# Kernel tuning notes

Measured on AMD Instinct MI355X. Metric: run time of the kernel, lower is better.

The kernel has to match this reference:

```python
import jax, jax.numpy as jnp
import numpy as np

N_NODES = 100000
N_EDGES = 1600000
D = 64
NUM_HOPS = 3


def setup_inputs() -> dict:
    key = jax.random.key(0)
    ks = jax.random.split(key, 8)
    return {
        "H_l": jax.random.normal(ks[0], (N_NODES, D), dtype=jnp.float32),
        "edge_row": jax.random.randint(ks[1], (N_EDGES,), 0, N_NODES, dtype=jnp.int64),
        "edge_col": jax.random.randint(ks[2], (N_EDGES,), 0, N_NODES, dtype=jnp.int64),
        "edge_val": jax.random.uniform(ks[3], (N_EDGES,), dtype=jnp.float32),
        "out_degree": jax.random.uniform(ks[4], (N_NODES,), dtype=jnp.float32),
        "in_degree": jax.random.uniform(ks[5], (N_NODES,), dtype=jnp.float32),
        "hop_attention": jnp.ones((NUM_HOPS,), dtype=jnp.float32),
        "theta_out": jnp.full((NUM_HOPS,), 0.5, dtype=jnp.float32),
        "theta_in": jnp.full((NUM_HOPS,), 0.5, dtype=jnp.float32),
        "Theta": jax.random.normal(ks[6], (D, D), dtype=jnp.float32) * (6.0 ** 0.5) / (2 * D) ** 0.5,
    }


def reference(H_l, edge_row, edge_col, edge_val, out_degree, in_degree,
              hop_attention, theta_out, theta_in, Theta):
    n = H_l.shape[0]
    num_hops = hop_attention.shape[0]
    alpha = jax.nn.softmax(hop_attention)

    def spmm(rows, cols, X):
        # (A @ X)[r] = sum over edges (r,c): val * X[c]
        return jax.ops.segment_sum(edge_val[:, None] * X[cols], rows, num_segments=n)

    # fixed degree-scaled features (degrees clamped as in __init__)
    X_out = jnp.maximum(out_degree, 1e-8)[:, None] * H_l
    X_in = jnp.maximum(in_degree, 1e-8)[:, None] * H_l
    sum_term = jnp.zeros_like(H_l)
    for k in range(num_hops):
        # A^{k+1} @ (D_out H) computed by one more application of A per hop
        X_out = spmm(edge_row, edge_col, X_out)
        # (A^{k+1})^T @ (D_in H): transpose swaps row/col roles
        X_in = spmm(edge_col, edge_row, X_in)
        sum_term = sum_term + alpha[k] * (theta_out[k] * X_out + theta_in[k] * X_in)

    conv_term = jax.nn.sigmoid(sum_term @ Theta)
    return conv_term + H_l
```

## Files before the change

kernel.cpp:

```cpp
#include <hip/hip_runtime.h>
#include <hip/hip_fp16.h>

#define DFEAT 64
#define BKT_SHIFT 8
#define BKT_NODES 256
#define NBMAX 512
#define CH 4096
#define SRC_BITS 18
#define SRC_MASK ((1 << SRC_BITS) - 1)

__device__ __forceinline__ unsigned short f2h(float f) {
    return __half_as_ushort(__float2half(f));
}
__device__ __forceinline__ float h2f(unsigned short u) {
    return __half2float(__ushort_as_half(u));
}

__global__ void init_kernel(const float* __restrict__ H,
                            const float* __restrict__ outdeg,
                            const float* __restrict__ indeg,
                            const float* __restrict__ hop_att,
                            const float* __restrict__ th_out,
                            const float* __restrict__ th_in,
                            unsigned short* __restrict__ XAout,
                            unsigned short* __restrict__ XAin,
                            float* __restrict__ coefs, int n4) {
    int idx = blockIdx.x * blockDim.x + threadIdx.x;
    if (idx == 0) {
        float m = fmaxf(fmaxf(hop_att[0], hop_att[1]), hop_att[2]);
        float e0 = __expf(hop_att[0] - m);
        float e1 = __expf(hop_att[1] - m);
        float e2 = __expf(hop_att[2] - m);
        float inv = 1.0f / (e0 + e1 + e2);
        coefs[0] = e0 * inv * th_out[0]; coefs[1] = e0 * inv * th_in[0];
        coefs[2] = e1 * inv * th_out[1]; coefs[3] = e1 * inv * th_in[1];
        coefs[4] = e2 * inv * th_out[2]; coefs[5] = e2 * inv * th_in[2];
    }
    if (idx >= n4) return;
    int row = idx >> 4;
    float4 h = reinterpret_cast<const float4*>(H)[idx];
    float doo = fmaxf(outdeg[row], 1e-8f);
    float dii = fmaxf(indeg[row], 1e-8f);
    reinterpret_cast<ushort4*>(XAout)[idx] =
        make_ushort4(f2h(h.x * doo), f2h(h.y * doo), f2h(h.z * doo), f2h(h.w * doo));
    reinterpret_cast<ushort4*>(XAin)[idx] =
        make_ushort4(f2h(h.x * dii), f2h(h.y * dii), f2h(h.z * dii), f2h(h.w * dii));
}

__global__ __launch_bounds__(256) void hist2d_kernel(
        const int* __restrict__ erow, const int* __restrict__ ecol,
        int* __restrict__ cnt2, int nEdges, int nB, int nBlkA) {
    __shared__ int hR[NBMAX], hC[NBMAX];
    int k = blockIdx.x;
    for (int i = threadIdx.x; i < nB; i += 256) { hR[i] = 0; hC[i] = 0; }
    __syncthreads();
    int base = k * CH;
    int nV = min(CH, nEdges - base);
    for (int i = threadIdx.x; i < nV; i += 256) {
        atomicAdd(&hR[erow[base + i] >> BKT_SHIFT], 1);
        atomicAdd(&hC[ecol[base + i] >> BKT_SHIFT], 1);
    }
    __syncthreads();
    for (int b = threadIdx.x; b < nB; b += 256) {
        cnt2[(size_t)b * nBlkA + k] = hR[b];
        cnt2[((size_t)nB + b) * nBlkA + k] = hC[b];
    }
}

__global__ void scan_reduce1(const int* __restrict__ p, int* __restrict__ bsum,
                             int n) {
    int t = threadIdx.x, lane = t & 63, wid = t >> 6;
    int base = blockIdx.x * 1024 + t * 4;
    int s = 0;
#pragma unroll
    for (int i = 0; i < 4; ++i) { int idx = base + i; if (idx < n) s += p[idx]; }
#pragma unroll
    for (int o = 32; o >= 1; o >>= 1) s += __shfl_down(s, o, 64);
    __shared__ int wsum[4];
    if (lane == 0) wsum[wid] = s;
    __syncthreads();
    if (t == 0) bsum[blockIdx.x] = wsum[0] + wsum[1] + wsum[2] + wsum[3];
}

__global__ void scan_spine1(int* __restrict__ bsum, int nChunks) {
    int lane = threadIdx.x;
    int carry = 0;
    for (int base = 0; base < nChunks; base += 64) {
        int i = base + lane;
        int v = (i < nChunks) ? bsum[i] : 0;
        int s = v;
#pragma unroll
        for (int o = 1; o < 64; o <<= 1) {
            int x = __shfl_up(s, o, 64);
            if (lane >= o) s += x;
        }
        if (i < nChunks) bsum[i] = carry + s - v;
        carry += __shfl(s, 63, 64);
    }
}

__global__ void scan_down1(int* __restrict__ p, const int* __restrict__ bsum,
                           int n) {
    int t = threadIdx.x, lane = t & 63, wid = t >> 6;
    int base = blockIdx.x * 1024 + t * 4;
    int v[4];
    int tsum = 0;
#pragma unroll
    for (int i = 0; i < 4; ++i) {
        v[i] = (base + i < n) ? p[base + i] : 0;
        tsum += v[i];
    }
    int inc = tsum;
#pragma unroll
    for (int o = 1; o < 64; o <<= 1) {
        int x = __shfl_up(inc, o, 64);
        if (lane >= o) inc += x;
    }
    __shared__ int wsum[4];
    if (lane == 63) wsum[wid] = inc;
    __syncthreads();
    int woff = 0;
    for (int w = 0; w < wid; ++w) woff += wsum[w];
    int run = bsum[blockIdx.x] + woff + inc - tsum;
#pragma unroll
    for (int i = 0; i < 4; ++i) {
        if (base + i < n) p[base + i] = run;
        run += v[i];
    }
}

__global__ __launch_bounds__(256) void partA_kernel(
        const int* __restrict__ erow, const int* __restrict__ ecol,
        const float* __restrict__ eval, const int* __restrict__ base2,
        int2* __restrict__ recR, int2* __restrict__ recC,
        int nEdges, int nB, int nBlkA) {
    __shared__ int hist[NBMAX], scn[NBMAX], cur[NBMAX], gbase[NBMAX];
    __shared__ unsigned short keybuf[CH], slotKey[CH];
    __shared__ int2 stage[CH];
    int dir = blockIdx.y;
    const int* dk = dir ? ecol : erow;
    const int* ds = dir ? erow : ecol;
    int2* rec = dir ? recC : recR;
    int k = blockIdx.x;
    int base = k * CH;
    int nV = min(CH, nEdges - base);
    for (int i = threadIdx.x; i < nB; i += 256) {
        hist[i] = 0; cur[i] = 0;
        gbase[i] = base2[((size_t)dir * nB + i) * nBlkA + k] - dir * nEdges;
    }
    __syncthreads();
    for (int i = threadIdx.x; i < nV; i += 256) {
        int key = dk[base + i] >> BKT_SHIFT;
        keybuf[i] = (unsigned short)key;
        atomicAdd(&hist[key], 1);
    }
    __syncthreads();
    if (threadIdx.x < 64) {
        int lane = threadIdx.x;
        int carry = 0;
        for (int bb = 0; bb < nB; bb += 64) {
            int i = bb + lane;
            int v = (i < nB) ? hist[i] : 0;
            int s = v;
#pragma unroll
            for (int o = 1; o < 64; o <<= 1) {
                int x = __shfl_up(s, o, 64);
                if (lane >= o) s += x;
            }
            if (i < nB) scn[i] = carry + s - v;
            carry += __shfl(s, 63, 64);
        }
    }
    __syncthreads();
    for (int i = threadIdx.x; i < nV; i += 256) {
        int e = base + i;
        int key = keybuf[i];
        int slot = scn[key] + atomicAdd(&cur[key], 1);
        int dl = dk[e] & (BKT_NODES - 1);
        stage[slot] = make_int2(ds[e] | (dl << SRC_BITS), __float_as_int(eval[e]));
        slotKey[slot] = (unsigned short)key;
    }
    __syncthreads();
    for (int i = threadIdx.x; i < nV; i += 256) {
        int key = slotKey[i];
        rec[gbase[key] + (i - scn[key])] = stage[i];
    }
}

__global__ __launch_bounds__(256) void partB_kernel(
        const int2* __restrict__ recR, const int2* __restrict__ recC,
        const int* __restrict__ base2,
        int* __restrict__ rowptr, int* __restrict__ colptr,
        unsigned* __restrict__ pairsR, unsigned* __restrict__ pairsC,
        int nEdges, int nB, int nBlkA, int nNodes) {
    __shared__ int hist[BKT_NODES], scn[BKT_NODES], cur[BKT_NODES];
    int dir = blockIdx.y;
    int b = blockIdx.x;
    const int2* rec = dir ? recC : recR;
    unsigned* pairs = dir ? pairsC : pairsR;
    int* nptr = dir ? colptr : rowptr;
    int segB = base2[((size_t)dir * nB + b) * nBlkA] - dir * nEdges;
    int segE = (b == nB - 1) ? nEdges
             : base2[((size_t)dir * nB + b + 1) * nBlkA] - dir * nEdges;
    int t = threadIdx.x;
    hist[t] = 0; cur[t] = 0;
    __syncthreads();
    for (int j = segB + t; j < segE; j += 256)
        atomicAdd(&hist[(rec[j].x >> SRC_BITS) & (BKT_NODES - 1)], 1);
    __syncthreads();
    if (t < 64) {
        int lane = t, carry = 0;
        for (int bb = 0; bb < BKT_NODES; bb += 64) {
            int i = bb + lane;
            int v = hist[i], s = v;
#pragma unroll
            for (int o = 1; o < 64; o <<= 1) {
                int x = __shfl_up(s, o, 64);
                if (lane >= o) s += x;
            }
            scn[i] = carry + s - v;
            carry += __shfl(s, 63, 64);
        }
    }
    __syncthreads();
    int node = (b << BKT_SHIFT) + t;
    if (node < nNodes) nptr[node] = segB + scn[t];
    if (b == nB - 1 && t == 0) nptr[nNodes] = nEdges;
    for (int j = segB + t; j < segE; j += 256) {
        int2 r = rec[j];
        int dl = (r.x >> SRC_BITS) & (BKT_NODES - 1);
        int slot = segB + scn[dl] + atomicAdd(&cur[dl], 1);
        unsigned vh = f2h(__int_as_float(r.y)) & 0x7FFFu;
        pairs[slot] = ((unsigned)(r.x & SRC_MASK) << 15) | vh;
    }
}

template <int FIRST, int LAST>
__global__ __launch_bounds__(256) void spmm_fused(
        const int* __restrict__ rowptr, const unsigned* __restrict__ pairsR,
        const int* __restrict__ colptr, const unsigned* __restrict__ pairsC,
        const __half* __restrict__ Xout, const __half* __restrict__ Xin,
        unsigned short* __restrict__ Yout, unsigned short* __restrict__ Yin,
        unsigned short* __restrict__ sumH, float* __restrict__ out,
        const float* __restrict__ H, const float* __restrict__ Theta,
        const float* __restrict__ coefs,
        int k, int nNodes) {
    __shared__ float Th[LAST ? 64 * 64 : 1];
    __shared__ float Srow[LAST ? 4 * 64 : 1];
    int wid = threadIdx.x >> 6;
    int lane = threadIdx.x & 63;
    int node = blockIdx.x * 4 + wid;
    bool live = node < nNodes;
    if (!LAST && !live) return;
    int nodeC = live ? node : 0;

    if (LAST) {
        for (int i = threadIdx.x; i < 64 * 64; i += 256) Th[i] = Theta[i];
    }

    float co = coefs[2 * k], ci = coefs[2 * k + 1];

    float accO, accI;
#pragma unroll
    for (int dir = 0; dir < 2; ++dir) {
        const unsigned* pairs = dir ? pairsC : pairsR;
        const __half* X = dir ? Xin : Xout;
        const int* ptr = dir ? colptr : rowptr;
        float a0 = 0.f, a1 = 0.f, a2 = 0.f, a3 = 0.f;
        float a4 = 0.f, a5 = 0.f, a6 = 0.f, a7 = 0.f;
        int b = ptr[nodeC], e = ptr[nodeC + 1];
        int j = b;
        for (; j + 8 <= e; j += 8) {
            unsigned p0 = pairs[j],     p1 = pairs[j + 1];
            unsigned p2 = pairs[j + 2], p3 = pairs[j + 3];
            unsigned p4 = pairs[j + 4], p5 = pairs[j + 5];
            unsigned p6 = pairs[j + 6], p7 = pairs[j + 7];
            float x0 = __half2float(X[(p0 >> 15) * DFEAT + lane]);
            float x1 = __half2float(X[(p1 >> 15) * DFEAT + lane]);
            float x2 = __half2float(X[(p2 >> 15) * DFEAT + lane]);
            float x3 = __half2float(X[(p3 >> 15) * DFEAT + lane]);
            float x4 = __half2float(X[(p4 >> 15) * DFEAT + lane]);
            float x5 = __half2float(X[(p5 >> 15) * DFEAT + lane]);
            float x6 = __half2float(X[(p6 >> 15) * DFEAT + lane]);
            float x7 = __half2float(X[(p7 >> 15) * DFEAT + lane]);
            a0 += h2f(p0 & 0x7FFFu) * x0;
            a1 += h2f(p1 & 0x7FFFu) * x1;
            a2 += h2f(p2 & 0x7FFFu) * x2;
            a3 += h2f(p3 & 0x7FFFu) * x3;
            a4 += h2f(p4 & 0x7FFFu) * x4;
            a5 += h2f(p5 & 0x7FFFu) * x5;
            a6 += h2f(p6 & 0x7FFFu) * x6;
            a7 += h2f(p7 & 0x7FFFu) * x7;
        }
        for (; j + 4 <= e; j += 4) {
            unsigned p0 = pairs[j],     p1 = pairs[j + 1];
            unsigned p2 = pairs[j + 2], p3 = pairs[j + 3];
            float x0 = __half2float(X[(p0 >> 15) * DFEAT + lane]);
            float x1 = __half2float(X[(p1 >> 15) * DFEAT + lane]);
            float x2 = __half2float(X[(p2 >> 15) * DFEAT + lane]);
            float x3 = __half2float(X[(p3 >> 15) * DFEAT + lane]);
            a0 += h2f(p0 & 0x7FFFu) * x0;
            a1 += h2f(p1 & 0x7FFFu) * x1;
            a2 += h2f(p2 & 0x7FFFu) * x2;
            a3 += h2f(p3 & 0x7FFFu) * x3;
        }
        for (; j < e; ++j) {
            unsigned p = pairs[j];
            a0 += h2f(p & 0x7FFFu) * __half2float(X[(p >> 15) * DFEAT + lane]);
        }
        float acc = ((a0 + a1) + (a2 + a3)) + ((a4 + a5) + (a6 + a7));
        if (dir == 0) accO = acc; else accI = acc;
    }

    int off = nodeC * DFEAT + lane;
    if (!LAST) {
        __builtin_nontemporal_store(f2h(accO), &Yout[off]);
        __builtin_nontemporal_store(f2h(accI), &Yin[off]);
        float s = co * accO + ci * accI;
        if (!FIRST) s += h2f(sumH[off]);
        __builtin_nontemporal_store(f2h(s), &sumH[off]);
    } else {
        float s = h2f(sumH[off]) + co * accO + ci * accI;
        __syncthreads();
        Srow[wid * 64 + lane] = s;
        float acc = 0.f;
#pragma unroll
        for (int kk = 0; kk < 64; ++kk)
            acc += Srow[wid * 64 + kk] * Th[kk * 64 + lane];
        if (live) {
            float r = 1.0f / (1.0f + __expf(-acc)) + H[off];
            __builtin_nontemporal_store(r, &out[off]);
        }
    }
}

extern "C" void kernel_launch(void* const* d_in, const int* in_sizes, int n_in,
                              void* d_out, int out_size, void* d_ws, size_t ws_size,
                              hipStream_t stream) {
    const float* H      = (const float*)d_in[0];
    const int*   erow   = (const int*)d_in[1];
    const int*   ecol   = (const int*)d_in[2];
    const float* eval   = (const float*)d_in[3];
    const float* outdeg = (const float*)d_in[4];
    const float* indeg  = (const float*)d_in[5];
    const float* hopatt = (const float*)d_in[6];
    const float* thout  = (const float*)d_in[7];
    const float* thin   = (const float*)d_in[8];
    const float* Theta  = (const float*)d_in[9];
    float* out = (float*)d_out;

    int nNodes = in_sizes[0] / DFEAT;
    int nEdges = in_sizes[1];

    char* ws = (char*)d_ws;
    size_t off = 0;
    auto alloc = [&](size_t bytes) {
        void* p = ws + off;
        off += (bytes + 255) & ~(size_t)255;
        return p;
    };
    size_t xBytes = (size_t)nNodes * DFEAT * sizeof(unsigned short);
    unsigned short* XAout = (unsigned short*)alloc(xBytes);
    unsigned short* XAin  = (unsigned short*)alloc(xBytes);
    unsigned short* XBout = (unsigned short*)alloc(xBytes);
    unsigned short* XBin  = (unsigned short*)alloc(xBytes);
    unsigned short* sumH  = (unsigned short*)alloc(xBytes);
    int*   rowptr = (int*)alloc((size_t)(nNodes + 1) * sizeof(int));
    int*   colptr = (int*)alloc((size_t)(nNodes + 1) * sizeof(int));
    int2*  recR   = (int2*)alloc((size_t)nEdges * sizeof(int2));
    int2*  recC   = (int2*)alloc((size_t)nEdges * sizeof(int2));
    unsigned* pairsR = (unsigned*)alloc((size_t)nEdges * sizeof(unsigned));
    unsigned* pairsC = (unsigned*)alloc((size_t)nEdges * sizeof(unsigned));

    int nB    = (nNodes + BKT_NODES - 1) >> BKT_SHIFT;
    int nBlkA = (nEdges + CH - 1) / CH;
    int L = 2 * nB * nBlkA;
    int nChunks = (L + 1023) / 1024;
    int*   cnt2 = (int*)alloc((size_t)L * sizeof(int));
    int*   bsum = (int*)alloc((size_t)nChunks * sizeof(int));
    float* coefs = (float*)alloc(8 * sizeof(float));

    int n4 = nNodes * (DFEAT / 4);
    int ewBlocks = (n4 + 255) / 256;
    int nodeBlocks = (nNodes + 3) / 4;

    init_kernel<<<ewBlocks, 256, 0, stream>>>(H, outdeg, indeg, hopatt, thout, thin,
                                              XAout, XAin, coefs, n4);
    hist2d_kernel<<<nBlkA, 256, 0, stream>>>(erow, ecol, cnt2, nEdges, nB, nBlkA);
    scan_reduce1<<<nChunks, 256, 0, stream>>>(cnt2, bsum, L);
    scan_spine1<<<1, 64, 0, stream>>>(bsum, nChunks);
    scan_down1<<<nChunks, 256, 0, stream>>>(cnt2, bsum, L);
    partA_kernel<<<dim3(nBlkA, 2), 256, 0, stream>>>(erow, ecol, eval, cnt2,
                                                     recR, recC, nEdges, nB, nBlkA);
    partB_kernel<<<dim3(nB, 2), 256, 0, stream>>>(recR, recC, cnt2,
                                                  rowptr, colptr, pairsR, pairsC,
                                                  nEdges, nB, nBlkA, nNodes);

    spmm_fused<1, 0><<<nodeBlocks, 256, 0, stream>>>(rowptr, pairsR, colptr, pairsC,
                                                     (const __half*)XAout, (const __half*)XAin,
                                                     XBout, XBin, sumH, nullptr,
                                                     nullptr, nullptr, coefs, 0, nNodes);
    spmm_fused<0, 0><<<nodeBlocks, 256, 0, stream>>>(rowptr, pairsR, colptr, pairsC,
                                                     (const __half*)XBout, (const __half*)XBin,
                                                     XAout, XAin, sumH, nullptr,
                                                     nullptr, nullptr, coefs, 1, nNodes);
    spmm_fused<0, 1><<<nodeBlocks, 256, 0, stream>>>(rowptr, pairsR, colptr, pairsC,
                                                     (const __half*)XAout, (const __half*)XAin,
                                                     nullptr, nullptr, sumH, out,
                                                     H, Theta, coefs, 2, nNodes);
}
```

Before: 431.2 us.

## Split SpMM directions into separate blocks with half2 gathers and separate final GEMM

```diff
diff --git a/kernel.cpp b/kernel.cpp
--- a/kernel.cpp
+++ b/kernel.cpp
@@ -236,102 +236,109 @@
 }
 
 template <int FIRST, int LAST>
-__global__ __launch_bounds__(256) void spmm_fused(
+__global__ __launch_bounds__(256) void spmm_split(
         const int* __restrict__ rowptr, const unsigned* __restrict__ pairsR,
         const int* __restrict__ colptr, const unsigned* __restrict__ pairsC,
         const __half* __restrict__ Xout, const __half* __restrict__ Xin,
         unsigned short* __restrict__ Yout, unsigned short* __restrict__ Yin,
-        unsigned short* __restrict__ sumH, float* __restrict__ out,
-        const float* __restrict__ H, const float* __restrict__ Theta,
-        const float* __restrict__ coefs,
-        int k, int nNodes) {
-    __shared__ float Th[LAST ? 64 * 64 : 1];
-    __shared__ float Srow[LAST ? 4 * 64 : 1];
+        unsigned short* __restrict__ sumO, unsigned short* __restrict__ sumI,
+        const float* __restrict__ coefs, int k, int nNodes) {
+    int b = blockIdx.x;
+    int slot = b & 7;
+    int dir = slot >> 2;
+    int g = (b >> 3) * 4 + (slot & 3);
     int wid = threadIdx.x >> 6;
     int lane = threadIdx.x & 63;
-    int node = blockIdx.x * 4 + wid;
-    bool live = node < nNodes;
-    if (!LAST && !live) return;
-    int nodeC = live ? node : 0;
-
-    if (LAST) {
-        for (int i = threadIdx.x; i < 64 * 64; i += 256) Th[i] = Theta[i];
-    }
-
-    float co = coefs[2 * k], ci = coefs[2 * k + 1];
-
-    float accO, accI;
-#pragma unroll
-    for (int dir = 0; dir < 2; ++dir) {
-        const unsigned* pairs = dir ? pairsC : pairsR;
-        const __half* X = dir ? Xin : Xout;
-        const int* ptr = dir ? colptr : rowptr;
-        float a0 = 0.f, a1 = 0.f, a2 = 0.f, a3 = 0.f;
-        float a4 = 0.f, a5 = 0.f, a6 = 0.f, a7 = 0.f;
-        int b = ptr[nodeC], e = ptr[nodeC + 1];
-        int j = b;
-        for (; j + 8 <= e; j += 8) {
-            unsigned p0 = pairs[j],     p1 = pairs[j + 1];
-            unsigned p2 = pairs[j + 2], p3 = pairs[j + 3];
-            unsigned p4 = pairs[j + 4], p5 = pairs[j + 5];
-            unsigned p6 = pairs[j + 6], p7 = pairs[j + 7];
-            float x0 = __half2float(X[(p0 >> 15) * DFEAT + lane]);
-            float x1 = __half2float(X[(p1 >> 15) * DFEAT + lane]);
-            float x2 = __half2float(X[(p2 >> 15) * DFEAT + lane]);
-            float x3 = __half2float(X[(p3 >> 15) * DFEAT + lane]);
-            float x4 = __half2float(X[(p4 >> 15) * DFEAT + lane]);
-            float x5 = __half2float(X[(p5 >> 15) * DFEAT + lane]);
-            float x6 = __half2float(X[(p6 >> 15) * DFEAT + lane]);
-            float x7 = __half2float(X[(p7 >> 15) * DFEAT + lane]);
-            a0 += h2f(p0 & 0x7FFFu) * x0;
-            a1 += h2f(p1 & 0x7FFFu) * x1;
-            a2 += h2f(p2 & 0x7FFFu) * x2;
-            a3 += h2f(p3 & 0x7FFFu) * x3;
-            a4 += h2f(p4 & 0x7FFFu) * x4;
-            a5 += h2f(p5 & 0x7FFFu) * x5;
-            a6 += h2f(p6 & 0x7FFFu) * x6;
-            a7 += h2f(p7 & 0x7FFFu) * x7;
-        }
-        for (; j + 4 <= e; j += 4) {
-            unsigned p0 = pairs[j],     p1 = pairs[j + 1];
-            unsigned p2 = pairs[j + 2], p3 = pairs[j + 3];
-            float x0 = __half2float(X[(p0 >> 15) * DFEAT + lane]);
-            float x1 = __half2float(X[(p1 >> 15) * DFEAT + lane]);
-            float x2 = __half2float(X[(p2 >> 15) * DFEAT + lane]);
-            float x3 = __half2float(X[(p3 >> 15) * DFEAT + lane]);
-            a0 += h2f(p0 & 0x7FFFu) * x0;
-            a1 += h2f(p1 & 0x7FFFu) * x1;
-            a2 += h2f(p2 & 0x7FFFu) * x2;
-            a3 += h2f(p3 & 0x7FFFu) * x3;
-        }
-        for (; j < e; ++j) {
-            unsigned p = pairs[j];
-            a0 += h2f(p & 0x7FFFu) * __half2float(X[(p >> 15) * DFEAT + lane]);
-        }
-        float acc = ((a0 + a1) + (a2 + a3)) + ((a4 + a5) + (a6 + a7));
-        if (dir == 0) accO = acc; else accI = acc;
-    }
-
-    int off = nodeC * DFEAT + lane;
-    if (!LAST) {
-        __builtin_nontemporal_store(f2h(accO), &Yout[off]);
-        __builtin_nontemporal_store(f2h(accI), &Yin[off]);
-        float s = co * accO + ci * accI;
-        if (!FIRST) s += h2f(sumH[off]);
-        __builtin_nontemporal_store(f2h(s), &sumH[off]);
-    } else {
-        float s = h2f(sumH[off]) + co * accO + ci * accI;
-        __syncthreads();
-        Srow[wid * 64 + lane] = s;
-        float acc = 0.f;
-#pragma unroll
-        for (int kk = 0; kk < 64; ++kk)
-            acc += Srow[wid * 64 + kk] * Th[kk * 64 + lane];
-        if (live) {
-            float r = 1.0f / (1.0f + __expf(-acc)) + H[off];
-            __builtin_nontemporal_store(r, &out[off]);
-        }
-    }
+    int node = g * 4 + wid;
+    if (node >= nNodes) return;
+
+    const int* ptr = dir ? colptr : rowptr;
+    const unsigned* pairs = dir ? pairsC : pairsR;
+    const __half* X = dir ? Xin : Xout;
+    unsigned short* Y = dir ? Yin : Yout;
+    unsigned short* sm = dir ? sumI : sumO;
+    float cf = coefs[2 * k + dir];
+
+    int hb = lane >> 5;
+    int sub = lane & 31;
+
+    float2 a0 = {0.f, 0.f}, a1 = {0.f, 0.f}, a2 = {0.f, 0.f}, a3 = {0.f, 0.f};
+    int bE = ptr[node], eE = ptr[node + 1];
+    int j = bE;
+    for (; j + 8 <= eE; j += 8) {
+        unsigned p0 = pairs[j     + hb];
+        unsigned p1 = pairs[j + 2 + hb];
+        unsigned p2 = pairs[j + 4 + hb];
+        unsigned p3 = pairs[j + 6 + hb];
+        float2 x0 = __half22float2(*(const __half2*)(X + (p0 >> 15) * DFEAT + 2 * sub));
+        float2 x1 = __half22float2(*(const __half2*)(X + (p1 >> 15) * DFEAT + 2 * sub));
+        float2 x2 = __half22float2(*(const __half2*)(X + (p2 >> 15) * DFEAT + 2 * sub));
+        float2 x3 = __half22float2(*(const __half2*)(X + (p3 >> 15) * DFEAT + 2 * sub));
+        float v0 = h2f(p0 & 0x7FFFu);
+        float v1 = h2f(p1 & 0x7FFFu);
+        float v2 = h2f(p2 & 0x7FFFu);
+        float v3 = h2f(p3 & 0x7FFFu);
+        a0.x += v0 * x0.x; a0.y += v0 * x0.y;
+        a1.x += v1 * x1.x; a1.y += v1 * x1.y;
+        a2.x += v2 * x2.x; a2.y += v2 * x2.y;
+        a3.x += v3 * x3.x; a3.y += v3 * x3.y;
+    }
+    if (j < eE) {
+#pragma unroll
+        for (int q = 0; q < 4; ++q) {
+            int idx = j + 2 * q + hb;
+            unsigned p = (idx < eE) ? pairs[idx] : 0u;
+            float2 x = __half22float2(*(const __half2*)(X + (p >> 15) * DFEAT + 2 * sub));
+            float v = h2f(p & 0x7FFFu);
+            a0.x += v * x.x; a0.y += v * x.y;
+        }
+    }
+    float ax = (a0.x + a1.x) + (a2.x + a3.x);
+    float ay = (a0.y + a1.y) + (a2.y + a3.y);
+    ax += __shfl_xor(ax, 32, 64);
+    ay += __shfl_xor(ay, 32, 64);
+
+    if (hb == 0) {
+        int off = node * DFEAT + 2 * sub;
+        if (!LAST) {
+            __half2 yv = __floats2half2_rn(ax, ay);
+            __builtin_nontemporal_store(*reinterpret_cast<unsigned*>(&yv),
+                                        reinterpret_cast<unsigned*>(Y + off));
+        }
+        float sx = cf * ax, sy = cf * ay;
+        if (!FIRST) {
+            __half2 old = *reinterpret_cast<const __half2*>(sm + off);
+            float2 of = __half22float2(old);
+            sx += of.x; sy += of.y;
+        }
+        __half2 sv = __floats2half2_rn(sx, sy);
+        __builtin_nontemporal_store(*reinterpret_cast<unsigned*>(&sv),
+                                    reinterpret_cast<unsigned*>(sm + off));
+    }
+}
+
+__global__ __launch_bounds__(256) void final_kernel(
+        const unsigned short* __restrict__ sumO,
+        const unsigned short* __restrict__ sumI,
+        const float* __restrict__ H, const float* __restrict__ Theta,
+        float* __restrict__ out, int nRows) {
+    __shared__ float Th[64 * 64];
+    __shared__ float Srow[4 * 64];
+    int t = threadIdx.x;
+    for (int i = t; i < 64 * 64; i += 256) Th[i] = Theta[i];
+    int rl = t >> 6;
+    int c = t & 63;
+    int row = blockIdx.x * 4 + rl;
+    int off = row * DFEAT + c;
+    float sv = (row < nRows) ? h2f(sumO[off]) + h2f(sumI[off]) : 0.f;
+    Srow[rl * 64 + c] = sv;
+    __syncthreads();
+    if (row >= nRows) return;
+    float acc = 0.f;
+#pragma unroll
+    for (int kk = 0; kk < 64; ++kk) acc += Srow[rl * 64 + kk] * Th[kk * 64 + c];
+    float r = 1.0f / (1.0f + __expf(-acc)) + H[off];
+    __builtin_nontemporal_store(r, &out[off]);
 }
 
 extern "C" void kernel_launch(void* const* d_in, const int* in_sizes, int n_in,
@@ -364,7 +371,8 @@
     unsigned short* XAin  = (unsigned short*)alloc(xBytes);
     unsigned short* XBout = (unsigned short*)alloc(xBytes);
     unsigned short* XBin  = (unsigned short*)alloc(xBytes);
-    unsigned short* sumH  = (unsigned short*)alloc(xBytes);
+    unsigned short* sumO  = (unsigned short*)alloc(xBytes);
+    unsigned short* sumI  = (unsigned short*)alloc(xBytes);
     int*   rowptr = (int*)alloc((size_t)(nNodes + 1) * sizeof(int));
     int*   colptr = (int*)alloc((size_t)(nNodes + 1) * sizeof(int));
     int2*  recR   = (int2*)alloc((size_t)nEdges * sizeof(int2));
@@ -382,7 +390,9 @@
 
     int n4 = nNodes * (DFEAT / 4);
     int ewBlocks = (n4 + 255) / 256;
-    int nodeBlocks = (nNodes + 3) / 4;
+    int gPerDir = (nNodes + 3) / 4;
+    int grid8 = (gPerDir + 3) / 4;
+    int splitGrid = 8 * grid8;
 
     init_kernel<<<ewBlocks, 256, 0, stream>>>(H, outdeg, indeg, hopatt, thout, thin,
                                               XAout, XAin, coefs, n4);
@@ -396,16 +406,19 @@
                                                   rowptr, colptr, pairsR, pairsC,
                                                   nEdges, nB, nBlkA, nNodes);
 
-    spmm_fused<1, 0><<<nodeBlocks, 256, 0, stream>>>(rowptr, pairsR, colptr, pairsC,
-                                                     (const __half*)XAout, (const __half*)XAin,
-                                                     XBout, XBin, sumH, nullptr,
-                                                     nullptr, nullptr, coefs, 0, nNodes);
-    spmm_fused<0, 0><<<nodeBlocks, 256, 0, stream>>>(rowptr, pairsR, colptr, pairsC,
-                                                     (const __half*)XBout, (const __half*)XBin,
-                                                     XAout, XAin, sumH, nullptr,
-                                                     nullptr, nullptr, coefs, 1, nNodes);
-    spmm_fused<0, 1><<<nodeBlocks, 256, 0, stream>>>(rowptr, pairsR, colptr, pairsC,
-                                                     (const __half*)XAout, (const __half*)XAin,
-                                                     nullptr, nullptr, sumH, out,
-                                                     H, Theta, coefs, 2, nNodes);
-}
+    spmm_split<1, 0><<<splitGrid, 256, 0, stream>>>(rowptr, pairsR, colptr, pairsC,
+                                                    (const __half*)XAout, (const __half*)XAin,
+                                                    XBout, XBin, sumO, sumI,
+                                                    coefs, 0, nNodes);
+    spmm_split<0, 0><<<splitGrid, 256, 0, stream>>>(rowptr, pairsR, colptr, pairsC,
+                                                    (const __half*)XBout, (const __half*)XBin,
+                                                    XAout, XAin, sumO, sumI,
+                                                    coefs, 1, nNodes);
+    spmm_split<0, 1><<<splitGrid, 256, 0, stream>>>(rowptr, pairsR, colptr, pairsC,
+                                                    (const __half*)XAout, (const __half*)XAin,
+                                                    nullptr, nullptr, sumO, sumI,
+                                                    coefs, 2, nNodes);
+
+    final_kernel<<<(nNodes + 3) / 4, 256, 0, stream>>>(sumO, sumI, H, Theta,
+                                                       out, nNodes);
+}
```

After: 462.8 us. +7.3%, slower.
